# Kernel tuning notes

Hardware: AMD Instinct MI355X
Metric: run time of the kernel (lower is better)

The kernel has to match this reference:

```python
import jax, jax.numpy as jnp
import numpy as np

B, C, T, H, W = 1024, 1, 500, 7, 7
HID, OUT = 16, 2


def setup_inputs() -> dict:
    key = jax.random.key(0)
    k1, k2, k3, k4 = jax.random.split(key, 4)
    rppg_embeddings = jax.random.normal(k1, (B, C, T, H, W), dtype=jnp.float32)
    rBr = jax.random.normal(k2, (B, C, T), dtype=jnp.float32)
    # final_dense_layer params: Linear(500,16) -> Dropout (identity at eval) -> Linear(16,2)
    W1 = jax.random.normal(k3, (C * T, HID), dtype=jnp.float32) / np.sqrt(C * T)
    b1 = jnp.zeros((HID,), dtype=jnp.float32)
    W2 = jax.random.normal(k4, (HID, OUT), dtype=jnp.float32) / np.sqrt(HID)
    b2 = jnp.zeros((OUT,), dtype=jnp.float32)
    return {"rppg_embeddings": rppg_embeddings, "rBr": rBr,
            "W1": W1, "b1": b1, "W2": W2, "b2": b2}


def reference(rppg_embeddings, rBr, W1, b1, W2, b2):
    # AvgPool3d(kernel=[1,7,7], stride=1, pad=0) on (B,C,T,7,7) -> (B,C,T,1,1):
    # equivalent to mean over the full 7x7 spatial window.
    x = jnp.mean(rppg_embeddings, axis=(-2, -1))            # (B, C, T)
    # batched FFT phase along time (replaces the per-(b,c) Python loop)
    phase = jnp.angle(jnp.fft.fft(x, axis=-1))              # (B, C, T)
    flat = phase.reshape(phase.shape[0], -1)                # (B, C*T) = (B, 500)
    h = flat @ W1 + b1                                      # (B, 16); dropout = identity (eval)
    rBP = h @ W2 + b2                                       # (B, 2)
    return rBP
```

## Files before the change

kernel.cpp:

```cpp
#include <hip/hip_runtime.h>
#include <math.h>

#ifndef M_PI
#define M_PI 3.14159265358979323846
#endif

#define T_LEN 500
#define HW49  49
#define HID   16
#define NOUT  2

__global__ __launch_bounds__(256) void pool_kernel(
    const float* __restrict__ rppg, float* __restrict__ xout)
{
    __shared__ __align__(16) float lds[12348];
    const int tid  = threadIdx.x;
    const int row  = blockIdx.x >> 1;
    const int half = blockIdx.x & 1;
    const int bin0 = half ? 252 : 0;
    const int nbin = half ? 248 : 252;
    const int nf4  = half ? 3038 : 3087;
    const float4* src = (const float4*)(rppg + (size_t)row * (T_LEN * HW49)
                                        + bin0 * HW49);
    float4* dst = (float4*)lds;
    #pragma unroll
    for (int s = 0; s < 13; ++s) {
        const int i = tid + 256 * s;
        if (i < nf4) dst[i] = src[i];
    }
    __syncthreads();
    if (tid < nbin) {
        const float* p = lds + tid * HW49;
        float acc = 0.f;
        #pragma unroll
        for (int j = 0; j < HW49; ++j) acc += p[j];
        xout[(size_t)row * T_LEN + bin0 + tid] = acc * (1.0f / 49.0f);
    }
}

__global__ __launch_bounds__(256, 4) void dft_head_kernel(
    const float* __restrict__ xin,
    const float* __restrict__ W1,
    const float* __restrict__ b1,
    const float* __restrict__ W2,
    const float* __restrict__ b2,
    float* __restrict__ out)
{
    __shared__ __align__(16) float xsh[512];
    __shared__ float wsum[4][HID + 1];
    const int tid = threadIdx.x;
    const int row = blockIdx.x;

    {
        float4* x4s = (float4*)xsh;
        const float4* xr4 = (const float4*)(xin + (size_t)row * T_LEN);
        if (tid < 125) x4s[tid] = xr4[tid];
        else if (tid < 128) x4s[tid] = float4{0.f, 0.f, 0.f, 0.f};
    }
    __syncthreads();

    float hp[HID];
    #pragma unroll
    for (int j = 0; j < HID; ++j) hp[j] = 0.f;

    if (tid <= 249) {
        const int k = tid;
        const double ang = (double)k * (-2.0 * M_PI / 500.0);
        double c1, s1;
        sincos(ang, &s1, &c1);
        const double c2 = fma(c1, c1, -(s1 * s1));
        const double s2 = 2.0 * c1 * s1;
        const float c1f = (float)c1, s1f = (float)s1;
        const float c2f = (float)c2, s2f = (float)s2;
        const float c3f = (float)fma(c1, c2, -(s1 * s2));
        const float s3f = (float)fma(c1, s2,  (s1 * c2));
        const float c4f = (float)fma(c2, c2, -(s2 * s2));
        const float s4f = (float)(2.0 * c2 * s2);

        float cw = 1.f, sw = 0.f;
        float re0 = 0.f, im0 = 0.f, re1 = 0.f, im1 = 0.f;
        float re2 = 0.f, im2 = 0.f, re3 = 0.f, im3 = 0.f;
        const float4* x4 = (const float4*)xsh;
        float4 xv = x4[0];
        for (int j = 0; j < 125; ++j) {
            const float4 nx = x4[j + 1];
            re0 = fmaf(xv.x, cw, re0); im0 = fmaf(xv.x, sw, im0);
            re1 = fmaf(xv.y, cw, re1); im1 = fmaf(xv.y, sw, im1);
            re2 = fmaf(xv.z, cw, re2); im2 = fmaf(xv.z, sw, im2);
            re3 = fmaf(xv.w, cw, re3); im3 = fmaf(xv.w, sw, im3);
            const float tc = fmaf(cw, c4f, -(sw * s4f));
            sw = fmaf(cw, s4f, sw * c4f);
            cw = tc;
            xv = nx;
        }
        const float re = re0 + fmaf(c1f, re1, -(s1f * im1))
                             + fmaf(c2f, re2, -(s2f * im2))
                             + fmaf(c3f, re3, -(s3f * im3));
        const float im = im0 + fmaf(c1f, im1,  (s1f * re1))
                             + fmaf(c2f, im2,  (s2f * re2))
                             + fmaf(c3f, im3,  (s3f * re3));
        const float ph = atan2f(im, re);

        if (k == 0) {
            const float* w = W1;
            #pragma unroll
            for (int j = 0; j < HID; ++j) hp[j] = ph * w[j];
        } else {
            const float* wa = W1 + k * HID;
            const float* wb = W1 + (T_LEN - k) * HID;
            #pragma unroll
            for (int j = 0; j < HID; ++j) hp[j] = ph * (wa[j] - wb[j]);
        }
    }

    #pragma unroll
    for (int j = 0; j < HID; ++j) {
        float v = hp[j];
        v += __shfl_xor(v, 1);  v += __shfl_xor(v, 2);
        v += __shfl_xor(v, 4);  v += __shfl_xor(v, 8);
        v += __shfl_xor(v, 16); v += __shfl_xor(v, 32);
        hp[j] = v;
    }
    if ((tid & 63) == 0) {
        const int w = tid >> 6;
        #pragma unroll
        for (int j = 0; j < HID; ++j) wsum[w][j] = hp[j];
    }
    __syncthreads();

    if (tid < NOUT) {
        const int o = tid;
        float acc = b2[o];
        #pragma unroll
        for (int j = 0; j < HID; ++j) {
            const float h = wsum[0][j] + wsum[1][j] + wsum[2][j] + wsum[3][j] + b1[j];
            acc = fmaf(h, W2[j * NOUT + o], acc);
        }
        out[row * NOUT + o] = acc;
    }
}

__global__ __launch_bounds__(256, 4) void bp_fused2_kernel(
    const float* __restrict__ rppg,
    const float* __restrict__ W1, const float* __restrict__ b1,
    const float* __restrict__ W2, const float* __restrict__ b2,
    float* __restrict__ out)
{
    __shared__ __align__(16) float stage[2][3136];
    __shared__ __align__(16) float xsh[512];
    __shared__ float wsum[4][HID + 1];
    const int tid = threadIdx.x;
    const int row = blockIdx.x;
    const float4* src4 = (const float4*)(rppg + (size_t)row * (T_LEN * HW49));

    if (tid < 12) xsh[T_LEN + tid] = 0.f;
    const float4 fz = {0.f, 0.f, 0.f, 0.f};
    float4 r0, r1, r2, r3;
    r0 = src4[tid]; r1 = src4[tid + 256]; r2 = src4[tid + 512];
    r3 = (tid < 16) ? src4[tid + 768] : fz;
    {
        float4* st = (float4*)stage[0];
        st[tid] = r0; st[tid + 256] = r1; st[tid + 512] = r2;
        if (tid < 16) st[tid + 768] = r3;
    }
    __syncthreads();
    const int bin  = tid >> 2;
    const int part = tid & 3;
    const int nels = (part < 3) ? 13 : 10;
    const int boff = bin * HW49 + part * 13;
    for (int c = 0; c < 8; ++c) {
        if (c < 7) {
            const int n4 = (c + 1 < 7) ? 784 : 637;
            const float4* b4 = src4 + 784 * (c + 1);
            r0 = (tid       < n4) ? b4[tid      ] : fz;
            r1 = (tid + 256 < n4) ? b4[tid + 256] : fz;
            r2 = (tid + 512 < n4) ? b4[tid + 512] : fz;
            r3 = (tid + 768 < n4) ? b4[tid + 768] : fz;
        }
        const int bins_c = (c < 7) ? 64 : 52;
        {
            const float* bufp = stage[c & 1];
            float s = 0.f;
            if (bin < bins_c) {
                const float* p = bufp + boff;
                for (int j = 0; j < nels; ++j) s += p[j];
            }
            s += __shfl_xor(s, 1);
            s += __shfl_xor(s, 2);
            if (part == 0 && bin < bins_c) xsh[c * 64 + bin] = s * (1.0f / 49.0f);
        }
        __syncthreads();
        if (c < 7) {
            const int n4 = (c + 1 < 7) ? 784 : 637;
            float4* st = (float4*)stage[(c + 1) & 1];
            if (tid       < n4) st[tid      ] = r0;
            if (tid + 256 < n4) st[tid + 256] = r1;
            if (tid + 512 < n4) st[tid + 512] = r2;
            if (tid + 768 < n4) st[tid + 768] = r3;
            __syncthreads();
        }
    }

    float hp[HID];
    #pragma unroll
    for (int j = 0; j < HID; ++j) hp[j] = 0.f;
    if (tid <= 249) {
        const int k = tid;
        const double ang = (double)k * (-2.0 * M_PI / 500.0);
        double c1, s1;
        sincos(ang, &s1, &c1);
        const double c2 = fma(c1, c1, -(s1 * s1));
        const double s2 = 2.0 * c1 * s1;
        const float c1f = (float)c1, s1f = (float)s1;
        const float c2f = (float)c2, s2f = (float)s2;
        const float c3f = (float)fma(c1, c2, -(s1 * s2));
        const float s3f = (float)fma(c1, s2,  (s1 * c2));
        const float c4f = (float)fma(c2, c2, -(s2 * s2));
        const float s4f = (float)(2.0 * c2 * s2);
        float cw = 1.f, sw = 0.f;
        float re0 = 0.f, im0 = 0.f, re1 = 0.f, im1 = 0.f;
        float re2 = 0.f, im2 = 0.f, re3 = 0.f, im3 = 0.f;
        const float4* x4 = (const float4*)xsh;
        float4 xv = x4[0];
        for (int j = 0; j < 125; ++j) {
            const float4 nx = x4[j + 1];
            re0 = fmaf(xv.x, cw, re0); im0 = fmaf(xv.x, sw, im0);
            re1 = fmaf(xv.y, cw, re1); im1 = fmaf(xv.y, sw, im1);
            re2 = fmaf(xv.z, cw, re2); im2 = fmaf(xv.z, sw, im2);
            re3 = fmaf(xv.w, cw, re3); im3 = fmaf(xv.w, sw, im3);
            const float tc = fmaf(cw, c4f, -(sw * s4f));
            sw = fmaf(cw, s4f, sw * c4f);
            cw = tc;
            xv = nx;
        }
        const float re = re0 + fmaf(c1f, re1, -(s1f * im1))
                             + fmaf(c2f, re2, -(s2f * im2))
                             + fmaf(c3f, re3, -(s3f * im3));
        const float im = im0 + fmaf(c1f, im1,  (s1f * re1))
                             + fmaf(c2f, im2,  (s2f * re2))
                             + fmaf(c3f, im3,  (s3f * re3));
        const float ph = atan2f(im, re);
        if (k == 0) {
            const float* w = W1;
            #pragma unroll
            for (int j = 0; j < HID; ++j) hp[j] = ph * w[j];
        } else {
            const float* wa = W1 + k * HID;
            const float* wb = W1 + (T_LEN - k) * HID;
            #pragma unroll
            for (int j = 0; j < HID; ++j) hp[j] = ph * (wa[j] - wb[j]);
        }
    }
    #pragma unroll
    for (int j = 0; j < HID; ++j) {
        float v = hp[j];
        v += __shfl_xor(v, 1);  v += __shfl_xor(v, 2);
        v += __shfl_xor(v, 4);  v += __shfl_xor(v, 8);
        v += __shfl_xor(v, 16); v += __shfl_xor(v, 32);
        hp[j] = v;
    }
    if ((tid & 63) == 0) {
        const int w = tid >> 6;
        #pragma unroll
        for (int j = 0; j < HID; ++j) wsum[w][j] = hp[j];
    }
    __syncthreads();
    if (tid < NOUT) {
        const int o = tid;
        float acc = b2[o];
        #pragma unroll
        for (int j = 0; j < HID; ++j) {
            const float h = wsum[0][j] + wsum[1][j] + wsum[2][j] + wsum[3][j] + b1[j];
            acc = fmaf(h, W2[j * NOUT + o], acc);
        }
        out[row * NOUT + o] = acc;
    }
}

extern "C" void kernel_launch(void* const* d_in, const int* in_sizes, int n_in,
                              void* d_out, int out_size, void* d_ws, size_t ws_size,
                              hipStream_t stream) {
    const float* rppg = (const float*)d_in[0];
    const float* W1 = (const float*)d_in[2];
    const float* b1 = (const float*)d_in[3];
    const float* W2 = (const float*)d_in[4];
    const float* b2 = (const float*)d_in[5];
    float* out = (float*)d_out;

    const size_t need = (size_t)1024 * T_LEN * sizeof(float);
    if (ws_size >= need) {
        float* x = (float*)d_ws;
        pool_kernel<<<dim3(2048), dim3(256), 0, stream>>>(rppg, x);
        dft_head_kernel<<<dim3(1024), dim3(256), 0, stream>>>(x, W1, b1, W2, b2, out);
    } else {
        bp_fused2_kernel<<<dim3(1024), dim3(256), 0, stream>>>(rppg, W1, b1, W2, b2, out);
    }
}
```

Measured before the change: 169.8 us.

## Use direct global-to-LDS loads with per-wave independent pooling in pool kernel

The pooling kernel now loads input through __builtin_amdgcn_global_load_lds, which writes straight into shared memory without going through registers. Blocks shrink to 128 threads, and each wave owns its own quarter-row slice of bins, so a wave only waits on its own loads with s_waitcnt and the block-wide barrier is gone. This targets register staging and barrier stalls in a memory-bound reduction. In exchange each thread sums two bins instead of one, and blocks are smaller, which changes occupancy.

New measurement: 168.9 us. About the same (-0.5%).

```diff
diff --git a/kernel.cpp b/kernel.cpp
--- a/kernel.cpp
+++ b/kernel.cpp
@@ -10,31 +10,47 @@
 #define HID   16
 #define NOUT  2
 
-__global__ __launch_bounds__(256) void pool_kernel(
+__global__ __launch_bounds__(128) void pool_kernel(
     const float* __restrict__ rppg, float* __restrict__ xout)
 {
     __shared__ __align__(16) float lds[12348];
     const int tid  = threadIdx.x;
+    const int wave = tid >> 6;
+    const int lane = tid & 63;
     const int row  = blockIdx.x >> 1;
     const int half = blockIdx.x & 1;
-    const int bin0 = half ? 252 : 0;
-    const int nbin = half ? 248 : 252;
-    const int nf4  = half ? 3038 : 3087;
-    const float4* src = (const float4*)(rppg + (size_t)row * (T_LEN * HW49)
-                                        + bin0 * HW49);
-    float4* dst = (float4*)lds;
-    #pragma unroll
-    for (int s = 0; s < 13; ++s) {
-        const int i = tid + 256 * s;
-        if (i < nf4) dst[i] = src[i];
-    }
-    __syncthreads();
-    if (tid < nbin) {
-        const float* p = lds + tid * HW49;
-        float acc = 0.f;
-        #pragma unroll
-        for (int j = 0; j < HW49; ++j) acc += p[j];
-        xout[(size_t)row * T_LEN + bin0 + tid] = acc * (1.0f / 49.0f);
+
+    const int bin0  = half ? (wave ? 376 : 252) : (wave ? 128 : 0);
+    const int nbin  = (half | wave) ? 124 : 128;
+    const int f4off = half ? (wave ? 4606 : 3087) : (wave ? 1568 : 0);
+    const int nf4   = (half | wave) ? 1519 : 1568;
+
+    const float4* g4 = (const float4*)(rppg + (size_t)row * (T_LEN * HW49)) + f4off;
+    float4* l4 = ((float4*)lds) + (wave ? 1568 : 0);
+
+    for (int call = 0; call * 64 < nf4; ++call) {
+        const int idx = call * 64 + lane;
+        if (idx < nf4) {
+            __builtin_amdgcn_global_load_lds(
+                (const __attribute__((address_space(1))) void*)(g4 + idx),
+                (__attribute__((address_space(3))) void*)(l4 + call * 64),
+                16, 0, 0);
+        }
+    }
+    __builtin_amdgcn_s_waitcnt(0);
+    __builtin_amdgcn_sched_barrier(0);
+
+    const float* base = (const float*)l4;
+    #pragma unroll
+    for (int rep = 0; rep < 2; ++rep) {
+        const int bin = rep * 64 + lane;
+        if (bin < nbin) {
+            const float* p = base + bin * HW49;
+            float s = 0.f;
+            #pragma unroll
+            for (int j = 0; j < HW49; ++j) s += p[j];
+            xout[(size_t)row * T_LEN + bin0 + bin] = s * (1.0f / 49.0f);
+        }
     }
 }
 
@@ -290,7 +306,7 @@
     const size_t need = (size_t)1024 * T_LEN * sizeof(float);
     if (ws_size >= need) {
         float* x = (float*)d_ws;
-        pool_kernel<<<dim3(2048), dim3(256), 0, stream>>>(rppg, x);
+        pool_kernel<<<dim3(2048), dim3(128), 0, stream>>>(rppg, x);
         dft_head_kernel<<<dim3(1024), dim3(256), 0, stream>>>(x, W1, b1, W2, b2, out);
     } else {
         bp_fused2_kernel<<<dim3(1024), dim3(256), 0, stream>>>(rppg, W1, b1, W2, b2, out);
```
